# Optimization experiments

Measured on AMD Instinct MI355X. Metric: run time of the kernel, lower is better.

Reference implementation:

```python
import jax, jax.numpy as jnp
import numpy as np

N_QUBITS = 12
DIM = 2 ** N_QUBITS  # 4096

_H = (jnp.array([[1.0, 1.0], [1.0, -1.0]]) / np.sqrt(2.0)).astype(jnp.complex64)
_X = jnp.array([[0.0, 1.0], [1.0, 0.0]], dtype=jnp.complex64)


def setup_inputs() -> dict:
    key = jax.random.key(0)
    k1, k2 = jax.random.split(key)
    state = jax.random.normal(k1, (8, 512, DIM), dtype=jnp.float32)
    params = jax.random.normal(k2, (N_QUBITS,), dtype=jnp.float32)
    return {"state": state, "params": params}


def _to_quantum(x):
    # faithful to _classical_to_quantum_inspired: normalize, phase = acos(|v|), sign * exp(i*phase)
    norms = jnp.linalg.norm(x, axis=-1, keepdims=True)
    v = x / (norms + 1e-8)
    mag = jnp.minimum(jnp.abs(v), 1.0)
    q = (jnp.sign(v) * jnp.exp(1j * jnp.arccos(mag))).astype(jnp.complex64)
    nrm = jnp.sqrt(jnp.sum(q.real ** 2 + q.imag ** 2, axis=-1, keepdims=True))
    return q / nrm.astype(jnp.complex64)


def _axis(q):
    # qubit q = bit q (LSB); tensor axes ordered MSB-first after batch axis 0
    return 1 + (N_QUBITS - 1 - q)


def _apply_1q(full, q, U):
    ax = _axis(q)
    moved = jnp.moveaxis(full, ax, -1)
    out = jnp.einsum('...b,ab->...a', moved, U)
    return jnp.moveaxis(out, -1, ax)


def _apply_ctrl(full, c, t, U):
    # apply U on target qubit t where control qubit c == 1
    axc = _axis(c)
    b0 = jnp.take(full, 0, axis=axc)
    b1 = jnp.take(full, 1, axis=axc)
    axt = _axis(t)
    axt_sub = axt - 1 if axt > axc else axt
    moved = jnp.moveaxis(b1, axt_sub, -1)
    b1n = jnp.moveaxis(jnp.einsum('...b,ab->...a', moved, U), -1, axt_sub)
    return jnp.stack([b0, b1n], axis=axc)


def _rx(theta):
    c = jnp.cos(theta / 2).astype(jnp.complex64)
    s = (-1j * jnp.sin(theta / 2)).astype(jnp.complex64)
    return jnp.stack([jnp.stack([c, s]), jnp.stack([s, c])])


def reference(state, params):
    B, T, D = state.shape
    psi = _to_quantum(state.reshape(B * T, D))  # (N, 2**n) complex64
    full = psi.reshape((B * T,) + (2,) * N_QUBITS)
    for q in range(N_QUBITS):
        full = _apply_1q(full, q, _H)                                  # Hadamard
        full = _apply_ctrl(full, q, (q + 1) % N_QUBITS, _rx(params[q]))  # controlled-RX
        if q < N_QUBITS - 1:
            full = _apply_ctrl(full, q, q + 1, _X)                     # CNOT
    amp = full.reshape(B * T, D)
    probs = amp.real ** 2 + amp.imag ** 2  # measurement probabilities
    return probs.reshape(B, T, D).astype(jnp.float32)
```

## Files before the change

### kernel.cpp

```cpp
#include <hip/hip_runtime.h>

#define NQ  12
#define DIM 4096
#define TPB 256

typedef float v2f __attribute__((ext_vector_type(2)));
typedef float v4f __attribute__((ext_vector_type(4)));


__device__ __forceinline__ float wave_reduce(float v) {
#pragma unroll
    for (int m = 32; m >= 1; m >>= 1) v += __shfl_xor(v, m, 64);
    return v;
}

#define BCAST(v, q) __uint_as_float(__builtin_amdgcn_readlane(__float_as_uint(v), (q)))

template <int MC, int MT, bool XGATE>
__device__ __forceinline__ void apply_layer(v2f* a, v2f ctv, v2f snv) {
#pragma unroll
    for (int i = 0; i < 16; ++i) {
        if (i & MC) continue;
        const int j = i | MC;
        const v2f t0 = a[i], t1 = a[j];
        a[i] = t0 + t1;
        a[j] = t0 - t1;
    }
#pragma unroll
    for (int i = 0; i < 16; ++i) {
        if (!(i & MC) || (i & MT)) continue;
        const int j = i | MT;
        const v2f b0 = a[i], b1 = a[j];
        const v2f s0 = snv * b0.yx;
        const v2f s1 = snv * b1.yx;
        if (XGATE) {
            a[i] = ctv * b1 + s0;
            a[j] = ctv * b0 + s1;
        } else {
            a[i] = ctv * b0 + s1;
            a[j] = ctv * b1 + s0;
        }
    }
}

__global__ __launch_bounds__(TPB, 4) void qlayer_kernel(
        const float* __restrict__ state, const float* __restrict__ params,
        float* __restrict__ out) {
    __shared__ __align__(16) v2f amp[DIM + 256];
    __shared__ float red[4];

    const int t = threadIdx.x;
    const int lane = t & 63;
    const long long sbase = (long long)blockIdx.x * DIM;

    const float th = params[lane < NQ ? lane : 0] * 0.5f;
    const float cl = cosf(th);
    const float sl = sinf(th);

    float x[16];
    const float4* gp = (const float4*)(state + sbase + t * 16);
    float ss = 0.f;
#pragma unroll
    for (int j = 0; j < 4; ++j) {
        const float4 v = gp[j];
        x[4 * j + 0] = v.x; x[4 * j + 1] = v.y;
        x[4 * j + 2] = v.z; x[4 * j + 3] = v.w;
        ss = fmaf(v.x, v.x, ss); ss = fmaf(v.y, v.y, ss);
        ss = fmaf(v.z, v.z, ss); ss = fmaf(v.w, v.w, ss);
    }
    ss = wave_reduce(ss);
    if (lane == 0) red[t >> 6] = ss;
    __syncthreads();
    const float nrm  = sqrtf(red[0] + red[1] + red[2] + red[3]);
    const float invd = 1.0f / (nrm + 1e-8f);

    v2f a[16];
#pragma unroll
    for (int k = 0; k < 16; ++k) {
        const float v   = x[k] * invd;
        const float re  = fminf(fmaxf(v, -1.0f), 1.0f);
        const float imb = sqrtf(fmaxf(1.0f - re * re, 0.f));
        const float im  = (v > 0.f) ? imb : ((v < 0.f) ? -imb : 0.f);
        v2f q; q.x = re; q.y = im;
        a[k] = q;
    }

#define CTV(q) ({ v2f _c; _c.x = BCAST(cl, q); _c.y = _c.x; _c; })
#define SNV(q) ({ float _s = BCAST(sl, q); v2f _v; _v.x = _s; _v.y = -_s; _v; })

    apply_layer<1, 2, true>(a, CTV(0), SNV(0));
    apply_layer<2, 4, true>(a, CTV(1), SNV(1));
    apply_layer<4, 8, true>(a, CTV(2), SNV(2));
    {
        const int p1base = 16 * t + 2 * (t >> 1);
#pragma unroll
        for (int k = 0; k < 8; ++k) {
            v4f w; w.x = a[2 * k].x; w.y = a[2 * k].y;
            w.z = a[2 * k + 1].x; w.w = a[2 * k + 1].y;
            *(v4f*)&amp[p1base + 2 * k] = w;
        }
    }
    __syncthreads();

    {
        const int p2base = (t & 7) + 136 * (t >> 3);
#pragma unroll
        for (int r = 0; r < 16; ++r)
            a[r] = amp[p2base + 8 * r + 2 * (r >> 2)];
        apply_layer<1, 2, true>(a, CTV(3), SNV(3));
        apply_layer<2, 4, true>(a, CTV(4), SNV(4));
        apply_layer<4, 8, true>(a, CTV(5), SNV(5));
#pragma unroll
        for (int r = 0; r < 16; ++r)
            amp[p2base + 8 * r + 2 * (r >> 2)] = a[r];
    }
    __syncthreads();

    {
        const int p3base = (t & 63) + 2 * ((t & 63) >> 5) + 1088 * (t >> 6);
#pragma unroll
        for (int r = 0; r < 16; ++r)
            a[r] = amp[p3base + 68 * r];
        apply_layer<1, 2, true>(a, CTV(6), SNV(6));
        apply_layer<2, 4, true>(a, CTV(7), SNV(7));
        apply_layer<4, 8, true>(a, CTV(8), SNV(8));
#pragma unroll
        for (int r = 0; r < 16; ++r)
            amp[p3base + 68 * r] = a[r];
    }
    __syncthreads();

    {
        const int p4base = 2 * t + 2 * (t >> 4);
#pragma unroll
        for (int k = 0; k < 8; ++k) {
            const v4f v = *(const v4f*)&amp[p4base + 544 * k];
            v2f q0; q0.x = v.x; q0.y = v.y;
            v2f q1; q1.x = v.z; q1.y = v.w;
            a[k] = q0;
            a[k + 8] = q1;
        }
        apply_layer<1, 2, true >(a, CTV(9),  SNV(9));
        apply_layer<2, 4, true >(a, CTV(10), SNV(10));
        apply_layer<4, 8, false>(a, CTV(11), SNV(11));

        const float scale = 0x1p-24f;
        float2* outp = (float2*)(out + sbase);
#pragma unroll
        for (int k = 0; k < 8; ++k) {
            const v2f q0 = a[k] * a[k];
            const v2f q1 = a[k | 8] * a[k | 8];
            outp[t + (k << 8)] = make_float2((q0.x + q0.y) * scale,
                                             (q1.x + q1.y) * scale);
        }
    }
#undef CTV
#undef SNV
}

extern "C" void kernel_launch(void* const* d_in, const int* in_sizes, int n_in,
                              void* d_out, int out_size, void* d_ws, size_t ws_size,
                              hipStream_t stream) {
    (void)in_sizes; (void)n_in; (void)out_size; (void)d_ws; (void)ws_size;
    const float* state  = (const float*)d_in[0];
    const float* params = (const float*)d_in[1];
    float* out = (float*)d_out;
    qlayer_kernel<<<dim3(4096), dim3(TPB), 0, stream>>>(state, params, out);
}
```

Before: 121.8 us.

## Replace padded LDS layout with XOR swizzle and raise occupancy target

```diff
diff --git a/kernel.cpp b/kernel.cpp
--- a/kernel.cpp
+++ b/kernel.cpp
@@ -43,11 +43,11 @@
     }
 }
 
-__global__ __launch_bounds__(TPB, 4) void qlayer_kernel(
+__global__ __launch_bounds__(TPB, 5) void qlayer_kernel(
         const float* __restrict__ state, const float* __restrict__ params,
         float* __restrict__ out) {
-    __shared__ __align__(16) v2f amp[DIM + 256];
-    __shared__ float red[4];
+    __shared__ __align__(16) v2f amp[DIM];
+    char* const lds = (char*)amp;
 
     const int t = threadIdx.x;
     const int lane = t & 63;
@@ -69,17 +69,19 @@
         ss = fmaf(v.z, v.z, ss); ss = fmaf(v.w, v.w, ss);
     }
     ss = wave_reduce(ss);
-    if (lane == 0) red[t >> 6] = ss;
+    if (lane == 0) ((float*)amp)[t >> 6] = ss;
     __syncthreads();
-    const float nrm  = sqrtf(red[0] + red[1] + red[2] + red[3]);
+    const float* redp = (const float*)amp;
+    const float nrm  = sqrtf(redp[0] + redp[1] + redp[2] + redp[3]);
     const float invd = 1.0f / (nrm + 1e-8f);
+    __syncthreads();
 
     v2f a[16];
 #pragma unroll
     for (int k = 0; k < 16; ++k) {
         const float v   = x[k] * invd;
         const float re  = fminf(fmaxf(v, -1.0f), 1.0f);
-        const float imb = sqrtf(fmaxf(1.0f - re * re, 0.f));
+        const float imb = __builtin_amdgcn_sqrtf(fmaxf(1.0f - re * re, 0.f));
         const float im  = (v > 0.f) ? imb : ((v < 0.f) ? -imb : 0.f);
         v2f q; q.x = re; q.y = im;
         a[k] = q;
@@ -92,49 +94,55 @@
     apply_layer<2, 4, true>(a, CTV(1), SNV(1));
     apply_layer<4, 8, true>(a, CTV(2), SNV(2));
     {
-        const int p1base = 16 * t + 2 * (t >> 1);
+        const int T1  = ((t >> 3) & 7) << 1;
+        const int v1b = (t << 7) + (T1 << 3);
 #pragma unroll
         for (int k = 0; k < 8; ++k) {
             v4f w; w.x = a[2 * k].x; w.y = a[2 * k].y;
             w.z = a[2 * k + 1].x; w.w = a[2 * k + 1].y;
-            *(v4f*)&amp[p1base + 2 * k] = w;
+            *(v4f*)(lds + (v1b ^ (k << 4))) = w;
         }
     }
     __syncthreads();
 
     {
-        const int p2base = (t & 7) + 136 * (t >> 3);
+        const int g   = t >> 3;
+        const int t8  = (g >> 2) & 1;
+        const int Bc  = ((t & 7) ^ ((g & 3) << 1)) + (g << 7);
+        const int A0b = (Bc + 8 * t8) << 3;
+        const int A1b = (Bc + 8 * (1 - t8)) << 3;
 #pragma unroll
         for (int r = 0; r < 16; ++r)
-            a[r] = amp[p2base + 8 * r + 2 * (r >> 2)];
+            a[r] = *(const v2f*)(lds + (((r & 1) ? A1b : A0b) + ((r >> 1) << 7)));
         apply_layer<1, 2, true>(a, CTV(3), SNV(3));
         apply_layer<2, 4, true>(a, CTV(4), SNV(4));
         apply_layer<4, 8, true>(a, CTV(5), SNV(5));
 #pragma unroll
         for (int r = 0; r < 16; ++r)
-            amp[p2base + 8 * r + 2 * (r >> 2)] = a[r];
+            *(v2f*)(lds + (((r & 1) ? A1b : A0b) + ((r >> 1) << 7))) = a[r];
     }
     __syncthreads();
 
     {
-        const int p3base = (t & 63) + 2 * ((t & 63) >> 5) + 1088 * (t >> 6);
+        const int b3b = ((t & 63) + ((t >> 6) << 10)) << 3;
 #pragma unroll
         for (int r = 0; r < 16; ++r)
-            a[r] = amp[p3base + 68 * r];
+            a[r] = *(const v2f*)(lds + ((b3b ^ ((r & 14) << 3)) + (r << 9)));
         apply_layer<1, 2, true>(a, CTV(6), SNV(6));
         apply_layer<2, 4, true>(a, CTV(7), SNV(7));
         apply_layer<4, 8, true>(a, CTV(8), SNV(8));
 #pragma unroll
         for (int r = 0; r < 16; ++r)
-            amp[p3base + 68 * r] = a[r];
+            *(v2f*)(lds + ((b3b ^ ((r & 14) << 3)) + (r << 9))) = a[r];
     }
     __syncthreads();
 
     {
-        const int p4base = 2 * t + 2 * (t >> 4);
+        const int wv  = t >> 6;
+        const int F0b = (t << 4) ^ (wv << 4);
 #pragma unroll
         for (int k = 0; k < 8; ++k) {
-            const v4f v = *(const v4f*)&amp[p4base + 544 * k];
+            const v4f v = *(const v4f*)(lds + ((F0b ^ ((k & 1) << 6)) + (k << 12)));
             v2f q0; q0.x = v.x; q0.y = v.y;
             v2f q1; q1.x = v.z; q1.y = v.w;
             a[k] = q0;
@@ -145,13 +153,14 @@
         apply_layer<4, 8, false>(a, CTV(11), SNV(11));
 
         const float scale = 0x1p-24f;
-        float2* outp = (float2*)(out + sbase);
+        v2f* outp = (v2f*)(out + sbase);
 #pragma unroll
         for (int k = 0; k < 8; ++k) {
             const v2f q0 = a[k] * a[k];
             const v2f q1 = a[k | 8] * a[k | 8];
-            outp[t + (k << 8)] = make_float2((q0.x + q0.y) * scale,
-                                             (q1.x + q1.y) * scale);
+            v2f res; res.x = (q0.x + q0.y) * scale;
+            res.y = (q1.x + q1.y) * scale;
+            __builtin_nontemporal_store(res, outp + t + (k << 8));
         }
     }
 #undef CTV
```

After: 126.0 us. +3.4%, slower.
